# Performance work log

Measured on AMD Instinct MI355X. Metric: run time of the kernel, lower is better.

The kernel has to match this reference:

```python
import jax, jax.numpy as jnp
import numpy as np

N_NODES = 100000
N_EDGES = 6400000
N_IN, E_HID, E_OUT = 768, 512, 256
HID, HEADS, N_CLASSES = 32, 2, 3
NEG_SLOPE = 0.2


def setup_inputs() -> dict:
    key = jax.random.key(0)
    ks = jax.random.split(key, 12)
    def glorot(k, shape):
        fan_in, fan_out = shape[0], shape[-1]
        lim = (6.0 / (fan_in + fan_out)) ** 0.5
        return jax.random.uniform(k, shape, jnp.float32, -lim, lim)
    return {
        "x": jax.random.normal(ks[0], (N_NODES, N_IN), jnp.float32),
        "edge_index": jax.random.randint(ks[1], (2, N_EDGES), 0, N_NODES, jnp.int64),
        "W_e1": glorot(ks[2], (N_IN, E_HID)),
        "b_e1": jnp.zeros((E_HID,), jnp.float32),
        "W_e2": glorot(ks[3], (E_HID, E_OUT)),
        "b_e2": jnp.zeros((E_OUT,), jnp.float32),
        "W_lin": glorot(ks[4], (E_OUT, HID)),
        "b_lin": jnp.zeros((HID,), jnp.float32),
        "W_att": glorot(ks[5], (HID, HEADS * N_CLASSES)),  # GATConv lin (no bias)
        "att_src": glorot(ks[6], (HEADS, N_CLASSES)),
        "att_dst": glorot(ks[7], (HEADS, N_CLASSES)),
        "bias": jnp.zeros((N_CLASSES,), jnp.float32),
    }


def reference(x, edge_index, W_e1, b_e1, W_e2, b_e2, W_lin, b_lin,
              W_att, att_src, att_dst, bias):
    # embedder (Linear-ReLU-Linear) then linear projection to hid
    h = jax.nn.relu(x @ W_e1 + b_e1)
    h = h @ W_e2 + b_e2
    h = h @ W_lin + b_lin                     # [N, hid]
    # GATConv(hid -> n_classes, heads=2, concat=False), add_self_loops=True
    N = h.shape[0]
    hh = (h @ W_att).reshape(N, HEADS, N_CLASSES)      # [N, H, C]
    a_src = jnp.sum(hh * att_src, axis=-1)             # [N, H]
    a_dst = jnp.sum(hh * att_dst, axis=-1)             # [N, H]
    loop = jnp.arange(N, dtype=edge_index.dtype)
    src = jnp.concatenate([edge_index[0], loop])       # [E+N]
    dst = jnp.concatenate([edge_index[1], loop])
    alpha = jax.nn.leaky_relu(a_src[src] + a_dst[dst], NEG_SLOPE)  # [E+N, H]
    # segment softmax over destination node (every segment nonempty via self-loops)
    amax = jax.ops.segment_max(alpha, dst, num_segments=N)
    alpha = jnp.exp(alpha - amax[dst])
    denom = jax.ops.segment_sum(alpha, dst, num_segments=N)
    alpha = alpha / denom[dst]                         # [E+N, H]
    msg = alpha[:, :, None] * hh[src]                  # [E+N, H, C]
    out = jax.ops.segment_sum(msg, dst, num_segments=N)  # [N, H, C]
    return out.mean(axis=1) + bias                     # concat=False -> mean over heads
```

## Files before the change

### kernel.cpp

```cpp
#include <hip/hip_runtime.h>


#define NNODES 100000
#define NEDGES 6400000
#define DIN    768
#define DH1    512
#define DH2    256
#define NEG_SLOPE 0.2f
#define LDSP   40
#define CHUNK  8192
#define NPART  782
#define NBUK   391

typedef __bf16 bf16x8 __attribute__((ext_vector_type(8)));
typedef float  f32x4  __attribute__((ext_vector_type(4)));

__device__ __forceinline__ float bf2f(unsigned short h) {
    return __uint_as_float(((unsigned)h) << 16);
}
__device__ __forceinline__ unsigned short f2bf(float f) {
    unsigned u = __float_as_uint(f);
    unsigned r = u + 0x7FFFu + ((u >> 16) & 1u);
    return (unsigned short)(r >> 16);
}
__device__ __forceinline__ float ldf(const void* p, int i, int isf32) {
    return isf32 ? ((const float*)p)[i] : bf2f(((const unsigned short*)p)[i]);
}
__device__ __forceinline__ uint4 packbf8(const float* p) {
    float4 u = *(const float4*)p;
    float4 v = *(const float4*)(p + 4);
    uint4 r;
    r.x = (unsigned)f2bf(u.x) | ((unsigned)f2bf(u.y) << 16);
    r.y = (unsigned)f2bf(u.z) | ((unsigned)f2bf(u.w) << 16);
    r.z = (unsigned)f2bf(v.x) | ((unsigned)f2bf(v.y) << 16);
    r.w = (unsigned)f2bf(v.z) | ((unsigned)f2bf(v.w) << 16);
    return r;
}

__global__ void detect_dtypes(const unsigned short* x, const unsigned short* we1,
                              const unsigned short* we2, const unsigned short* wlin,
                              const unsigned short* watt, const int* ei, int* flags) {
    __shared__ int cnt;
    int b = blockIdx.x, t = threadIdx.x;
    if (t == 0) cnt = 0;
    __syncthreads();
    if (b < 5) {
        const unsigned short* p = (b == 0) ? x : (b == 1) ? we1 : (b == 2) ? we2
                                  : (b == 3) ? wlin : watt;
        int K = (b == 4) ? 96 : 512;
        int c = 0;
        for (int i = t; i < K; i += 256) {
            int e = (p[2 * i] >> 7) & 0xFF;
            if (e >= 0x66 && e <= 0x8C) c++;
        }
        atomicAdd(&cnt, c);
        __syncthreads();
        if (t == 0) flags[b] = (cnt * 10 < K * 6) ? 1 : 0;
    } else {
        int c = 0;
        for (int i = t; i < 2048; i += 256)
            if (ei[2 * i + 1] != 0) c++;
        atomicAdd(&cnt, c);
        __syncthreads();
        if (t == 0) { flags[5] = (cnt == 0) ? 1 : 0; flags[15] = 0; }
    }
}

__global__ void transpose_conv(const void* in, unsigned short* out, int K, int N,
                               const int* flags, int fidx) {
    int f32 = flags[fidx];
    int idx = blockIdx.x * 256 + threadIdx.x;
    if (idx >= K * N) return;
    int k = idx / N, n = idx - k * N;
    unsigned short v = f32 ? f2bf(((const float*)in)[idx])
                           : ((const unsigned short*)in)[idx];
    out[(size_t)n * K + k] = v;
}

template <bool RELU>
__global__ __launch_bounds__(256)
void gemm_bt(const void* __restrict__ A,
             const unsigned short* __restrict__ Bt,
             const unsigned short* __restrict__ bias,
             unsigned short* __restrict__ C,
             int M, int K, int N, const int* flags, int aidx, int nt_n) {
    __shared__ unsigned short sA[128 * LDSP];
    __shared__ unsigned short sB[128 * LDSP];
    const int af32 = flags[aidx];
    const int tid = threadIdx.x;

    const int nwg = gridDim.x;
    const int bid = blockIdx.x;
    const int xcd = bid & 7, bidx = bid >> 3;
    const int q = nwg >> 3, r = nwg & 7;
    const int logical = (xcd < r ? xcd * (q + 1) : r * (q + 1) + (xcd - r) * q) + bidx;
    const int m0 = (logical / nt_n) * 128;
    const int n0 = (logical % nt_n) * 128;

    const int srow = tid >> 2;
    const int scol = (tid & 3) * 8;
    int ar0 = m0 + srow;      if (ar0 >= M) ar0 = M - 1;
    int ar1 = m0 + 64 + srow; if (ar1 >= M) ar1 = M - 1;
    const unsigned short* Ah = (const unsigned short*)A;
    const float*          Af = (const float*)A;
    const unsigned short* gA0h = Ah + (size_t)ar0 * K + scol;
    const unsigned short* gA1h = Ah + (size_t)ar1 * K + scol;
    const float*          gA0f = Af + (size_t)ar0 * K + scol;
    const float*          gA1f = Af + (size_t)ar1 * K + scol;
    const unsigned short* gB0 = Bt + (size_t)(n0 + srow) * K + scol;
    const unsigned short* gB1 = Bt + (size_t)(n0 + 64 + srow) * K + scol;

    const int wave = tid >> 6, lane = tid & 63;
    const int wr = wave >> 1, wc = wave & 1;
    const int lr = lane & 15;
    const int lk = (lane >> 4) * 8;
    f32x4 acc[4][4] = {};

    for (int k0 = 0; k0 < K; k0 += 32) {
        uint4 a0, a1;
        if (af32) { a0 = packbf8(gA0f + k0); a1 = packbf8(gA1f + k0); }
        else      { a0 = *(const uint4*)(gA0h + k0); a1 = *(const uint4*)(gA1h + k0); }
        uint4 b0 = *(const uint4*)(gB0 + k0);
        uint4 b1 = *(const uint4*)(gB1 + k0);
        __syncthreads();
        *(uint4*)&sA[srow * LDSP + scol]        = a0;
        *(uint4*)&sA[(64 + srow) * LDSP + scol] = a1;
        *(uint4*)&sB[srow * LDSP + scol]        = b0;
        *(uint4*)&sB[(64 + srow) * LDSP + scol] = b1;
        __syncthreads();
        bf16x8 aF[4], bF[4];
#pragma unroll
        for (int i = 0; i < 4; i++) aF[i] = *(const bf16x8*)&sA[(wr * 64 + i * 16 + lr) * LDSP + lk];
#pragma unroll
        for (int j = 0; j < 4; j++) bF[j] = *(const bf16x8*)&sB[(wc * 64 + j * 16 + lr) * LDSP + lk];
#pragma unroll
        for (int i = 0; i < 4; i++)
#pragma unroll
            for (int j = 0; j < 4; j++)
                acc[i][j] = __builtin_amdgcn_mfma_f32_16x16x32_bf16(aF[i], bF[j], acc[i][j], 0, 0, 0);
    }

    float bv[4];
#pragma unroll
    for (int j = 0; j < 4; j++) bv[j] = bf2f(bias[n0 + wc * 64 + j * 16 + lr]);
#pragma unroll
    for (int i = 0; i < 4; i++) {
        int rbase = m0 + wr * 64 + i * 16 + (lane >> 4) * 4;
#pragma unroll
        for (int r = 0; r < 4; r++) {
            int row = rbase + r;
            if (row < M) {
                size_t base = (size_t)row * N + n0 + wc * 64 + lr;
#pragma unroll
                for (int j = 0; j < 4; j++) {
                    float v = acc[i][j][r] + bv[j];
                    if (RELU) v = fmaxf(v, 0.f);
                    C[base + j * 16] = f2bf(v);
                }
            }
        }
    }
}

__global__ __launch_bounds__(256)
void node_att(const unsigned short* __restrict__ h2,
              const void* __restrict__ Wlin,
              const unsigned short* __restrict__ blin,
              const void* __restrict__ Watt,
              const void* __restrict__ attS,
              const void* __restrict__ attD,
              float* __restrict__ hh, float* __restrict__ asrc,
              float* __restrict__ adst, const int* flags) {
    __shared__ float sW[256 * 32];
    __shared__ float sh2[8 * 256];
    __shared__ float sH[8 * 32];
    __shared__ float sHH[8 * 6];
    const int wlf = flags[3], waf = flags[4];
    const int tid = threadIdx.x;
    for (int i = tid; i < 256 * 32; i += 256) sW[i] = ldf(Wlin, i, wlf);
    const int n0 = blockIdx.x * 8;
    {
        int e = tid * 8;
        int r = e >> 8;
        int c = e & 255;
        uint4 v = *(const uint4*)(h2 + (size_t)(n0 + r) * 256 + c);
        float* o = &sh2[r * 256 + c];
        o[0] = __uint_as_float(v.x << 16); o[1] = __uint_as_float(v.x & 0xFFFF0000u);
        o[2] = __uint_as_float(v.y << 16); o[3] = __uint_as_float(v.y & 0xFFFF0000u);
        o[4] = __uint_as_float(v.z << 16); o[5] = __uint_as_float(v.z & 0xFFFF0000u);
        o[6] = __uint_as_float(v.w << 16); o[7] = __uint_as_float(v.w & 0xFFFF0000u);
    }
    __syncthreads();
    const int nl = tid >> 5;
    const int c  = tid & 31;
    float acc = bf2f(blin[c]);
    const float* hrow = &sh2[nl * 256];
#pragma unroll 8
    for (int k = 0; k < 256; k++) acc += hrow[k] * sW[k * 32 + c];
    sH[nl * 32 + c] = acc;
    __syncthreads();
    if (tid < 48) {
        int n = tid / 6, j = tid - (tid / 6) * 6;
        float s = 0.f;
#pragma unroll
        for (int k = 0; k < 32; k++) s += sH[n * 32 + k] * ldf(Watt, k * 6 + j, waf);
        sHH[n * 6 + j] = s;
        hh[(size_t)(n0 + n) * 6 + j] = s;
    }
    __syncthreads();
    if (tid < 16) {
        int n = tid >> 1, hd = tid & 1;
        float s = 0.f, d = 0.f;
#pragma unroll
        for (int cc = 0; cc < 3; cc++) {
            float v = sHH[n * 6 + hd * 3 + cc];
            s += v * ldf(attS, hd * 3 + cc, waf);
            d += v * ldf(attD, hd * 3 + cc, waf);
        }
        asrc[(size_t)(n0 + n) * 2 + hd] = s;
        adst[(size_t)(n0 + n) * 2 + hd] = d;
    }
}


__global__ __launch_bounds__(256)
void part_hist(const int* __restrict__ ei, unsigned* __restrict__ histG,
               const int* __restrict__ flags) {
    __shared__ unsigned h[NBUK];
    int k = blockIdx.x, t = threadIdx.x;
    for (int i = t; i < NBUK; i += 256) h[i] = 0;
    __syncthreads();
    int e0 = k * CHUNK;
    int e1 = e0 + CHUNK; if (e1 > NEDGES) e1 = NEDGES;
    int i64 = flags[5];
    for (int e = e0 + t; e < e1; e += 256) {
        int d = i64 ? (int)((const long long*)ei)[NEDGES + e] : ei[NEDGES + e];
        atomicAdd(&h[d >> 8], 1u);
    }
    __syncthreads();
    for (int i = t; i < NBUK; i += 256) histG[(size_t)i * NPART + k] = h[i];
}

__global__ __launch_bounds__(256)
void part_scan(const unsigned* __restrict__ histG, unsigned* __restrict__ start,
               unsigned* __restrict__ btot) {
    int b = blockIdx.x, t = threadIdx.x;
    const unsigned* col = histG + (size_t)b * NPART;
    unsigned* out = start + (size_t)b * NPART;
    unsigned v[4]; unsigned sum = 0;
#pragma unroll
    for (int i = 0; i < 4; i++) {
        int k = t * 4 + i;
        unsigned x = (k < NPART) ? col[k] : 0;
        v[i] = x; sum += x;
    }
    __shared__ unsigned s[256];
    s[t] = sum; __syncthreads();
    for (int off = 1; off < 256; off <<= 1) {
        unsigned x = (t >= off) ? s[t - off] : 0;
        __syncthreads();
        s[t] += x;
        __syncthreads();
    }
    unsigned ex = s[t] - sum;
    unsigned run = ex;
#pragma unroll
    for (int i = 0; i < 4; i++) {
        int k = t * 4 + i;
        if (k < NPART) out[k] = run;
        run += v[i];
    }
    if (t == 255) btot[b] = s[255];
}

__global__ void bucket_base(const unsigned* __restrict__ btot, unsigned* __restrict__ bbase) {
    __shared__ unsigned s[512];
    int t = threadIdx.x;
    unsigned v = (t < NBUK) ? btot[t] : 0;
    s[t] = v;
    __syncthreads();
    for (int off = 1; off < 512; off <<= 1) {
        unsigned x = (t >= off) ? s[t - off] : 0;
        __syncthreads();
        s[t] += x;
        __syncthreads();
    }
    if (t < NBUK) bbase[t] = s[t] - v;
    if (t == NBUK - 1) bbase[NBUK] = s[t];
}

__global__ __launch_bounds__(256)
void part_scatter(const int* __restrict__ ei, const unsigned* __restrict__ start,
                  const unsigned* __restrict__ bbase, uint2* __restrict__ pairs,
                  const int* __restrict__ flags) {
    __shared__ unsigned cur[NBUK];
    int k = blockIdx.x, t = threadIdx.x;
    for (int i = t; i < NBUK; i += 256)
        cur[i] = bbase[i] + start[(size_t)i * NPART + k];
    __syncthreads();
    int e0 = k * CHUNK;
    int e1 = e0 + CHUNK; if (e1 > NEDGES) e1 = NEDGES;
    int i64 = flags[5];
    for (int e = e0 + t; e < e1; e += 256) {
        int s, d;
        if (i64) {
            const long long* E = (const long long*)ei;
            s = (int)E[e];
            d = (int)E[NEDGES + e];
        } else {
            s = ei[e];
            d = ei[NEDGES + e];
        }
        unsigned pos = atomicAdd(&cur[d >> 8], 1u);
        pairs[pos] = make_uint2((unsigned)s, (unsigned)d);
    }
}

__global__ __launch_bounds__(256)
void bucket_csr(const uint2* __restrict__ pairs, const unsigned* __restrict__ bbase,
                int* __restrict__ count, int* __restrict__ offs,
                int* __restrict__ sorted) {
    int b = blockIdx.x, t = threadIdx.x;
    unsigned e0 = bbase[b], e1 = bbase[b + 1];
    int d0n = b << 8;
    int nd = NNODES - d0n; if (nd > 256) nd = 256;
    __shared__ unsigned cnt[256], s[256], cur[256];
    cnt[t] = 0;
    __syncthreads();
    for (unsigned e = e0 + t; e < e1; e += 256)
        atomicAdd(&cnt[pairs[e].y & 255], 1u);
    __syncthreads();
    unsigned myc = cnt[t];
    s[t] = myc; __syncthreads();
    for (int off = 1; off < 256; off <<= 1) {
        unsigned x = (t >= off) ? s[t - off] : 0;
        __syncthreads();
        s[t] += x;
        __syncthreads();
    }
    unsigned ex = s[t] - myc;
    if (t < nd) {
        count[d0n + t] = (int)myc;
        offs[d0n + t]  = (int)(e0 + ex);
    }
    cur[t] = e0 + ex;
    __syncthreads();
    for (unsigned e = e0 + t; e < e1; e += 256) {
        uint2 p = pairs[e];
        unsigned pos = atomicAdd(&cur[p.y & 255], 1u);
        sorted[pos] = (int)p.x;
    }
}

__global__ __launch_bounds__(256)
void gather_finalize(const int* __restrict__ sorted, const int* __restrict__ offs,
                     const int* __restrict__ count,
                     const float* __restrict__ asrc, const float* __restrict__ adst,
                     const float* __restrict__ hh,
                     const unsigned short* __restrict__ bias,
                     void* __restrict__ out, const int* __restrict__ flags) {
    int w = blockIdx.x * 4 + (threadIdx.x >> 6);
    if (w >= NNODES) return;
    int lane = threadIdx.x & 63;
    int base = offs[w];
    int cnt  = count[w];
    float2 ad = *(const float2*)(adst + 2 * (size_t)w);

    float d0 = 0.f, d1 = 0.f;
    float n0 = 0.f, n1 = 0.f, n2 = 0.f, n3 = 0.f, n4 = 0.f, n5 = 0.f;
    for (int k = lane; k < cnt; k += 64) {
        int s = sorted[base + k];
        float2 as = *(const float2*)(asrc + 2 * (size_t)s);
        float a0 = as.x + ad.x; a0 = a0 > 0.f ? a0 : NEG_SLOPE * a0;
        float a1 = as.y + ad.y; a1 = a1 > 0.f ? a1 : NEG_SLOPE * a1;
        float p0 = __expf(fminf(a0, 60.f));
        float p1 = __expf(fminf(a1, 60.f));
        const float* hs = hh + 6 * (size_t)s;
        d0 += p0; d1 += p1;
        n0 += p0 * hs[0]; n1 += p0 * hs[1]; n2 += p0 * hs[2];
        n3 += p1 * hs[3]; n4 += p1 * hs[4]; n5 += p1 * hs[5];
    }
#pragma unroll
    for (int m = 32; m > 0; m >>= 1) {
        d0 += __shfl_xor(d0, m, 64); d1 += __shfl_xor(d1, m, 64);
        n0 += __shfl_xor(n0, m, 64); n1 += __shfl_xor(n1, m, 64);
        n2 += __shfl_xor(n2, m, 64); n3 += __shfl_xor(n3, m, 64);
        n4 += __shfl_xor(n4, m, 64); n5 += __shfl_xor(n5, m, 64);
    }
    if (lane == 0) {
        float2 as = *(const float2*)(asrc + 2 * (size_t)w);
        float a0 = as.x + ad.x; a0 = a0 > 0.f ? a0 : NEG_SLOPE * a0;
        float a1 = as.y + ad.y; a1 = a1 > 0.f ? a1 : NEG_SLOPE * a1;
        float p0 = __expf(fminf(a0, 60.f));
        float p1 = __expf(fminf(a1, 60.f));
        const float* hw = hh + 6 * (size_t)w;
        d0 += p0; d1 += p1;
        n0 += p0 * hw[0]; n1 += p0 * hw[1]; n2 += p0 * hw[2];
        n3 += p1 * hw[3]; n4 += p1 * hw[4]; n5 += p1 * hw[5];

        float o0 = 0.5f * (n0 / d0 + n3 / d1) + bf2f(bias[0]);
        float o1 = 0.5f * (n1 / d0 + n4 / d1) + bf2f(bias[1]);
        float o2 = 0.5f * (n2 / d0 + n5 / d1) + bf2f(bias[2]);
        if (flags[0]) {
            float* o = (float*)out;
            o[3 * (size_t)w + 0] = o0; o[3 * (size_t)w + 1] = o1; o[3 * (size_t)w + 2] = o2;
        } else {
            unsigned short* o = (unsigned short*)out;
            o[3 * (size_t)w + 0] = f2bf(o0); o[3 * (size_t)w + 1] = f2bf(o1); o[3 * (size_t)w + 2] = f2bf(o2);
        }
    }
}

extern "C" void kernel_launch(void* const* d_in, const int* in_sizes, int n_in,
                              void* d_out, int out_size, void* d_ws, size_t ws_size,
                              hipStream_t stream) {
    const unsigned short* x    = (const unsigned short*)d_in[0];
    const int*            ei   = (const int*)d_in[1];
    const unsigned short* We1  = (const unsigned short*)d_in[2];
    const unsigned short* be1  = (const unsigned short*)d_in[3];
    const unsigned short* We2  = (const unsigned short*)d_in[4];
    const unsigned short* be2  = (const unsigned short*)d_in[5];
    const unsigned short* Wlin = (const unsigned short*)d_in[6];
    const unsigned short* blin = (const unsigned short*)d_in[7];
    const unsigned short* Watt = (const unsigned short*)d_in[8];
    const unsigned short* attS = (const unsigned short*)d_in[9];
    const unsigned short* attD = (const unsigned short*)d_in[10];
    const unsigned short* bias = (const unsigned short*)d_in[11];

    char* ws = (char*)d_ws;
    unsigned short* W1t   = (unsigned short*)(ws + 0);
    unsigned short* W2t   = (unsigned short*)(ws + 786432);
    unsigned short* h2    = (unsigned short*)(ws + 1048576);
    float*    hh    = (float*)(ws + 52248576);
    float*    asrc  = (float*)(ws + 54648576);
    float*    adst  = (float*)(ws + 55448576);
    int*      count = (int*)(ws + 56248576);
    int*      offs  = (int*)(ws + 56648576);
    unsigned* btot  = (unsigned*)(ws + 57048576);
    unsigned* bbase = (unsigned*)(ws + 57052672);
    int*      flags = (int*)(ws + 59448576);
    unsigned short* h1 = (unsigned short*)(ws + 59448640);
    uint2*    pairs  = (uint2*)(ws + 59448640);
    int*      sorted = (int*)(ws + 110648640);
    unsigned* histG  = (unsigned*)(ws + 136248640);
    unsigned* start  = (unsigned*)(ws + 137471744);
    (void)ws_size; (void)in_sizes; (void)n_in; (void)out_size;

    detect_dtypes<<<6, 256, 0, stream>>>(x, We1, We2, Wlin, Watt, ei, flags);

    transpose_conv<<<(DIN * DH1 + 255) / 256, 256, 0, stream>>>(We1, W1t, DIN, DH1, flags, 1);
    transpose_conv<<<(DH1 * DH2 + 255) / 256, 256, 0, stream>>>(We2, W2t, DH1, DH2, flags, 2);

    dim3 blk(256);
    int nwg1 = ((NNODES + 127) / 128) * (DH1 / 128);
    gemm_bt<true><<<nwg1, blk, 0, stream>>>(x, W1t, be1, h1, NNODES, DIN, DH1,
                                            flags, 0, DH1 / 128);
    int nwg2 = ((NNODES + 127) / 128) * (DH2 / 128);
    gemm_bt<false><<<nwg2, blk, 0, stream>>>(h1, W2t, be2, h2, NNODES, DH1, DH2,
                                             flags, 15, DH2 / 128);

    node_att<<<NNODES / 8, 256, 0, stream>>>(h2, Wlin, blin, Watt, attS, attD,
                                             hh, asrc, adst, flags);

    part_hist<<<NPART, 256, 0, stream>>>(ei, histG, flags);
    part_scan<<<NBUK, 256, 0, stream>>>(histG, start, btot);
    bucket_base<<<1, 512, 0, stream>>>(btot, bbase);
    part_scatter<<<NPART, 256, 0, stream>>>(ei, start, bbase, pairs, flags);
    bucket_csr<<<NBUK, 256, 0, stream>>>(pairs, bbase, count, offs, sorted);
    gather_finalize<<<(NNODES + 3) / 4, 256, 0, stream>>>(sorted, offs, count,
                                                          asrc, adst, hh, bias,
                                                          d_out, flags);
}
```

Baseline: 1.061 ms.

## Replace CSR sort with bucket LDS-atomic accumulation and use direct-to-LDS GEMM loads

The per-destination CSR build (bucket_csr) and the gather kernel are replaced by bucket_acc. It accumulates softmax numerators and denominators in shared-memory atomics per 256-node bucket, splits each bucket across 8 sub-blocks, and merges the partial sums in combine_out. Edge pairs are packed into one 32-bit word (src<<8 | local dst), and the per-node source data is packed into an 8-float record so a gather needs two float4 loads. The bf16 GEMM path now uses global_load_lds to copy tiles straight into a k-major LDS layout. In exchange it adds LDS atomic contention and a partial buffer of 8×N×8 floats that must be written and reduced.

```diff
diff --git a/kernel.cpp b/kernel.cpp
--- a/kernel.cpp
+++ b/kernel.cpp
@@ -7,10 +7,10 @@
 #define DH1    512
 #define DH2    256
 #define NEG_SLOPE 0.2f
-#define LDSP   40
 #define CHUNK  8192
 #define NPART  782
 #define NBUK   391
+#define SSUB   8
 
 typedef __bf16 bf16x8 __attribute__((ext_vector_type(8)));
 typedef float  f32x4  __attribute__((ext_vector_type(4)));
@@ -35,6 +35,11 @@
     r.z = (unsigned)f2bf(v.x) | ((unsigned)f2bf(v.y) << 16);
     r.w = (unsigned)f2bf(v.z) | ((unsigned)f2bf(v.w) << 16);
     return r;
+}
+__device__ __forceinline__ void gload16(const unsigned short* g, unsigned short* l) {
+    __builtin_amdgcn_global_load_lds(
+        (const __attribute__((address_space(1))) unsigned int*)g,
+        (__attribute__((address_space(3))) unsigned int*)l, 16, 0, 0);
 }
 
 __global__ void detect_dtypes(const unsigned short* x, const unsigned short* we1,
@@ -84,8 +89,8 @@
              const unsigned short* __restrict__ bias,
              unsigned short* __restrict__ C,
              int M, int K, int N, const int* flags, int aidx, int nt_n) {
-    __shared__ unsigned short sA[128 * LDSP];
-    __shared__ unsigned short sB[128 * LDSP];
+    __shared__ unsigned short sA[4096];
+    __shared__ unsigned short sB[4096];
     const int af32 = flags[aidx];
     const int tid = threadIdx.x;
 
@@ -97,42 +102,53 @@
     const int m0 = (logical / nt_n) * 128;
     const int n0 = (logical % nt_n) * 128;
 
+    const int wave = tid >> 6, lane = tid & 63;
+
     const int srow = tid >> 2;
-    const int scol = (tid & 3) * 8;
+    const int c4   = tid & 3;
     int ar0 = m0 + srow;      if (ar0 >= M) ar0 = M - 1;
     int ar1 = m0 + 64 + srow; if (ar1 >= M) ar1 = M - 1;
-    const unsigned short* Ah = (const unsigned short*)A;
-    const float*          Af = (const float*)A;
-    const unsigned short* gA0h = Ah + (size_t)ar0 * K + scol;
-    const unsigned short* gA1h = Ah + (size_t)ar1 * K + scol;
-    const float*          gA0f = Af + (size_t)ar0 * K + scol;
-    const float*          gA1f = Af + (size_t)ar1 * K + scol;
-    const unsigned short* gB0 = Bt + (size_t)(n0 + srow) * K + scol;
-    const unsigned short* gB1 = Bt + (size_t)(n0 + 64 + srow) * K + scol;
-
-    const int wave = tid >> 6, lane = tid & 63;
+    const float* gA0f = (const float*)A + (size_t)ar0 * K + c4 * 8;
+    const float* gA1f = (const float*)A + (size_t)ar1 * K + c4 * 8;
+    unsigned short* swA0 = &sA[(c4 * 128 + srow) * 8];
+    unsigned short* swA1 = &sA[(c4 * 128 + 64 + srow) * 8];
+
+    const int grow = ((wave & 1) << 6) + lane;
+    int arow = m0 + grow; if (arow >= M) arow = M - 1;
+    const unsigned short* gAl1 = (const unsigned short*)A + (size_t)arow * K + (wave >> 1) * 8;
+    const unsigned short* gAl2 = gAl1 + 16;
+    const unsigned short* gBl1 = Bt + (size_t)(n0 + grow) * K + (wave >> 1) * 8;
+    const unsigned short* gBl2 = gBl1 + 16;
+    unsigned short* ldsA1 = &sA[wave * 512];
+    unsigned short* ldsA2 = &sA[2048 + wave * 512];
+    unsigned short* ldsB1 = &sB[wave * 512];
+    unsigned short* ldsB2 = &sB[2048 + wave * 512];
+
     const int wr = wave >> 1, wc = wave & 1;
     const int lr = lane & 15;
-    const int lk = (lane >> 4) * 8;
+    const int aBase = ((lane >> 4) * 128 + wr * 64 + lr) * 8;
+    const int bBase = ((lane >> 4) * 128 + wc * 64 + lr) * 8;
     f32x4 acc[4][4] = {};
 
     for (int k0 = 0; k0 < K; k0 += 32) {
         uint4 a0, a1;
         if (af32) { a0 = packbf8(gA0f + k0); a1 = packbf8(gA1f + k0); }
-        else      { a0 = *(const uint4*)(gA0h + k0); a1 = *(const uint4*)(gA1h + k0); }
-        uint4 b0 = *(const uint4*)(gB0 + k0);
-        uint4 b1 = *(const uint4*)(gB1 + k0);
-        __syncthreads();
-        *(uint4*)&sA[srow * LDSP + scol]        = a0;
-        *(uint4*)&sA[(64 + srow) * LDSP + scol] = a1;
-        *(uint4*)&sB[srow * LDSP + scol]        = b0;
-        *(uint4*)&sB[(64 + srow) * LDSP + scol] = b1;
+        __syncthreads();
+        if (af32) {
+            *(uint4*)swA0 = a0;
+            *(uint4*)swA1 = a1;
+        } else {
+            gload16(gAl1 + k0, ldsA1);
+            gload16(gAl2 + k0, ldsA2);
+        }
+        gload16(gBl1 + k0, ldsB1);
+        gload16(gBl2 + k0, ldsB2);
         __syncthreads();
         bf16x8 aF[4], bF[4];
 #pragma unroll
-        for (int i = 0; i < 4; i++) aF[i] = *(const bf16x8*)&sA[(wr * 64 + i * 16 + lr) * LDSP + lk];
-#pragma unroll
-        for (int j = 0; j < 4; j++) bF[j] = *(const bf16x8*)&sB[(wc * 64 + j * 16 + lr) * LDSP + lk];
+        for (int i = 0; i < 4; i++) aF[i] = *(const bf16x8*)&sA[aBase + i * 128];
+#pragma unroll
+        for (int j = 0; j < 4; j++) bF[j] = *(const bf16x8*)&sB[bBase + j * 128];
 #pragma unroll
         for (int i = 0; i < 4; i++)
 #pragma unroll
@@ -147,13 +163,13 @@
     for (int i = 0; i < 4; i++) {
         int rbase = m0 + wr * 64 + i * 16 + (lane >> 4) * 4;
 #pragma unroll
-        for (int r = 0; r < 4; r++) {
-            int row = rbase + r;
+        for (int r2 = 0; r2 < 4; r2++) {
+            int row = rbase + r2;
             if (row < M) {
                 size_t base = (size_t)row * N + n0 + wc * 64 + lr;
 #pragma unroll
                 for (int j = 0; j < 4; j++) {
-                    float v = acc[i][j][r] + bv[j];
+                    float v = acc[i][j][r2] + bv[j];
                     if (RELU) v = fmaxf(v, 0.f);
                     C[base + j * 16] = f2bf(v);
                 }
@@ -169,8 +185,8 @@
               const void* __restrict__ Watt,
               const void* __restrict__ attS,
               const void* __restrict__ attD,
-              float* __restrict__ hh, float* __restrict__ asrc,
-              float* __restrict__ adst, const int* flags) {
+              float* __restrict__ spack, float* __restrict__ adst,
+              const int* flags) {
     __shared__ float sW[256 * 32];
     __shared__ float sh2[8 * 256];
     __shared__ float sH[8 * 32];
@@ -205,7 +221,6 @@
 #pragma unroll
         for (int k = 0; k < 32; k++) s += sH[n * 32 + k] * ldf(Watt, k * 6 + j, waf);
         sHH[n * 6 + j] = s;
-        hh[(size_t)(n0 + n) * 6 + j] = s;
     }
     __syncthreads();
     if (tid < 16) {
@@ -217,8 +232,12 @@
             s += v * ldf(attS, hd * 3 + cc, waf);
             d += v * ldf(attD, hd * 3 + cc, waf);
         }
-        asrc[(size_t)(n0 + n) * 2 + hd] = s;
         adst[(size_t)(n0 + n) * 2 + hd] = d;
+        spack[(size_t)(n0 + n) * 8 + hd] = s;
+    }
+    if (tid < 48) {
+        int n = tid / 6, j = tid - (tid / 6) * 6;
+        spack[(size_t)(n0 + n) * 8 + 2 + j] = sHH[n * 6 + j];
     }
 }
 
@@ -291,7 +310,7 @@
 
 __global__ __launch_bounds__(256)
 void part_scatter(const int* __restrict__ ei, const unsigned* __restrict__ start,
-                  const unsigned* __restrict__ bbase, uint2* __restrict__ pairs,
+                  const unsigned* __restrict__ bbase, unsigned* __restrict__ pairs,
                   const int* __restrict__ flags) {
     __shared__ unsigned cur[NBUK];
     int k = blockIdx.x, t = threadIdx.x;
@@ -312,102 +331,81 @@
             d = ei[NEDGES + e];
         }
         unsigned pos = atomicAdd(&cur[d >> 8], 1u);
-        pairs[pos] = make_uint2((unsigned)s, (unsigned)d);
-    }
-}
-
-__global__ __launch_bounds__(256)
-void bucket_csr(const uint2* __restrict__ pairs, const unsigned* __restrict__ bbase,
-                int* __restrict__ count, int* __restrict__ offs,
-                int* __restrict__ sorted) {
-    int b = blockIdx.x, t = threadIdx.x;
-    unsigned e0 = bbase[b], e1 = bbase[b + 1];
+        pairs[pos] = ((unsigned)s << 8) | (unsigned)(d & 255);
+    }
+}
+
+__global__ __launch_bounds__(256)
+void bucket_acc(const unsigned* __restrict__ pairs, const unsigned* __restrict__ bbase,
+                const float* __restrict__ spack, const float* __restrict__ adst,
+                float* __restrict__ partial) {
+    __shared__ float acc[256 * 8];
+    __shared__ float sad[512];
+    int b = blockIdx.x, s = blockIdx.y, t = threadIdx.x;
     int d0n = b << 8;
     int nd = NNODES - d0n; if (nd > 256) nd = 256;
-    __shared__ unsigned cnt[256], s[256], cur[256];
-    cnt[t] = 0;
-    __syncthreads();
-    for (unsigned e = e0 + t; e < e1; e += 256)
-        atomicAdd(&cnt[pairs[e].y & 255], 1u);
-    __syncthreads();
-    unsigned myc = cnt[t];
-    s[t] = myc; __syncthreads();
-    for (int off = 1; off < 256; off <<= 1) {
-        unsigned x = (t >= off) ? s[t - off] : 0;
-        __syncthreads();
-        s[t] += x;
-        __syncthreads();
-    }
-    unsigned ex = s[t] - myc;
-    if (t < nd) {
-        count[d0n + t] = (int)myc;
-        offs[d0n + t]  = (int)(e0 + ex);
-    }
-    cur[t] = e0 + ex;
-    __syncthreads();
-    for (unsigned e = e0 + t; e < e1; e += 256) {
-        uint2 p = pairs[e];
-        unsigned pos = atomicAdd(&cur[p.y & 255], 1u);
-        sorted[pos] = (int)p.x;
-    }
-}
-
-__global__ __launch_bounds__(256)
-void gather_finalize(const int* __restrict__ sorted, const int* __restrict__ offs,
-                     const int* __restrict__ count,
-                     const float* __restrict__ asrc, const float* __restrict__ adst,
-                     const float* __restrict__ hh,
-                     const unsigned short* __restrict__ bias,
-                     void* __restrict__ out, const int* __restrict__ flags) {
-    int w = blockIdx.x * 4 + (threadIdx.x >> 6);
-    if (w >= NNODES) return;
-    int lane = threadIdx.x & 63;
-    int base = offs[w];
-    int cnt  = count[w];
-    float2 ad = *(const float2*)(adst + 2 * (size_t)w);
-
-    float d0 = 0.f, d1 = 0.f;
-    float n0 = 0.f, n1 = 0.f, n2 = 0.f, n3 = 0.f, n4 = 0.f, n5 = 0.f;
-    for (int k = lane; k < cnt; k += 64) {
-        int s = sorted[base + k];
-        float2 as = *(const float2*)(asrc + 2 * (size_t)s);
-        float a0 = as.x + ad.x; a0 = a0 > 0.f ? a0 : NEG_SLOPE * a0;
-        float a1 = as.y + ad.y; a1 = a1 > 0.f ? a1 : NEG_SLOPE * a1;
+    for (int i = t; i < 2048; i += 256) acc[i] = 0.f;
+    for (int i = t; i < 2 * nd; i += 256) sad[i] = adst[(size_t)d0n * 2 + i];
+    unsigned e0 = bbase[b], e1 = bbase[b + 1];
+    unsigned per = (e1 - e0 + SSUB - 1) / SSUB;
+    unsigned s0 = e0 + s * per;
+    unsigned s1 = s0 + per; if (s1 > e1) s1 = e1;
+    __syncthreads();
+    for (unsigned e = s0 + t; e < s1; e += 256) {
+        unsigned p = pairs[e];
+        unsigned src = p >> 8, dl = p & 255u;
+        float4 q0 = *(const float4*)(spack + 8 * (size_t)src);
+        float4 q1 = *(const float4*)(spack + 8 * (size_t)src + 4);
+        float a0 = q0.x + sad[2 * dl];     a0 = a0 > 0.f ? a0 : NEG_SLOPE * a0;
+        float a1 = q0.y + sad[2 * dl + 1]; a1 = a1 > 0.f ? a1 : NEG_SLOPE * a1;
         float p0 = __expf(fminf(a0, 60.f));
         float p1 = __expf(fminf(a1, 60.f));
-        const float* hs = hh + 6 * (size_t)s;
-        d0 += p0; d1 += p1;
-        n0 += p0 * hs[0]; n1 += p0 * hs[1]; n2 += p0 * hs[2];
-        n3 += p1 * hs[3]; n4 += p1 * hs[4]; n5 += p1 * hs[5];
-    }
-#pragma unroll
-    for (int m = 32; m > 0; m >>= 1) {
-        d0 += __shfl_xor(d0, m, 64); d1 += __shfl_xor(d1, m, 64);
-        n0 += __shfl_xor(n0, m, 64); n1 += __shfl_xor(n1, m, 64);
-        n2 += __shfl_xor(n2, m, 64); n3 += __shfl_xor(n3, m, 64);
-        n4 += __shfl_xor(n4, m, 64); n5 += __shfl_xor(n5, m, 64);
-    }
-    if (lane == 0) {
-        float2 as = *(const float2*)(asrc + 2 * (size_t)w);
-        float a0 = as.x + ad.x; a0 = a0 > 0.f ? a0 : NEG_SLOPE * a0;
-        float a1 = as.y + ad.y; a1 = a1 > 0.f ? a1 : NEG_SLOPE * a1;
-        float p0 = __expf(fminf(a0, 60.f));
-        float p1 = __expf(fminf(a1, 60.f));
-        const float* hw = hh + 6 * (size_t)w;
-        d0 += p0; d1 += p1;
-        n0 += p0 * hw[0]; n1 += p0 * hw[1]; n2 += p0 * hw[2];
-        n3 += p1 * hw[3]; n4 += p1 * hw[4]; n5 += p1 * hw[5];
-
-        float o0 = 0.5f * (n0 / d0 + n3 / d1) + bf2f(bias[0]);
-        float o1 = 0.5f * (n1 / d0 + n4 / d1) + bf2f(bias[1]);
-        float o2 = 0.5f * (n2 / d0 + n5 / d1) + bf2f(bias[2]);
-        if (flags[0]) {
-            float* o = (float*)out;
-            o[3 * (size_t)w + 0] = o0; o[3 * (size_t)w + 1] = o1; o[3 * (size_t)w + 2] = o2;
-        } else {
-            unsigned short* o = (unsigned short*)out;
-            o[3 * (size_t)w + 0] = f2bf(o0); o[3 * (size_t)w + 1] = f2bf(o1); o[3 * (size_t)w + 2] = f2bf(o2);
-        }
+        float* a = &acc[dl * 8];
+        atomicAdd(&a[0], p0);
+        atomicAdd(&a[1], p1);
+        atomicAdd(&a[2], p0 * q0.z);
+        atomicAdd(&a[3], p0 * q0.w);
+        atomicAdd(&a[4], p0 * q1.x);
+        atomicAdd(&a[5], p1 * q1.y);
+        atomicAdd(&a[6], p1 * q1.z);
+        atomicAdd(&a[7], p1 * q1.w);
+    }
+    __syncthreads();
+    float* dst = partial + ((size_t)s * NNODES + d0n) * 8;
+    for (int i = t; i < nd * 8; i += 256) dst[i] = acc[i];
+}
+
+__global__ void combine_out(const float* __restrict__ partial, const float* __restrict__ spack,
+                            const float* __restrict__ adst,
+                            const unsigned short* __restrict__ bias,
+                            void* __restrict__ out, const int* __restrict__ flags) {
+    int n = blockIdx.x * 256 + threadIdx.x;
+    if (n >= NNODES) return;
+    float v[8] = {0.f, 0.f, 0.f, 0.f, 0.f, 0.f, 0.f, 0.f};
+    for (int s = 0; s < SSUB; s++) {
+        const float* p = partial + ((size_t)s * NNODES + n) * 8;
+#pragma unroll
+        for (int j = 0; j < 8; j++) v[j] += p[j];
+    }
+    float4 q0 = *(const float4*)(spack + 8 * (size_t)n);
+    float4 q1 = *(const float4*)(spack + 8 * (size_t)n + 4);
+    float2 ad = *(const float2*)(adst + 2 * (size_t)n);
+    float a0 = q0.x + ad.x; a0 = a0 > 0.f ? a0 : NEG_SLOPE * a0;
+    float a1 = q0.y + ad.y; a1 = a1 > 0.f ? a1 : NEG_SLOPE * a1;
+    float p0 = __expf(fminf(a0, 60.f));
+    float p1 = __expf(fminf(a1, 60.f));
+    v[0] += p0; v[1] += p1;
+    v[2] += p0 * q0.z; v[3] += p0 * q0.w; v[4] += p0 * q1.x;
+    v[5] += p1 * q1.y; v[6] += p1 * q1.z; v[7] += p1 * q1.w;
+    float o0 = 0.5f * (v[2] / v[0] + v[5] / v[1]) + bf2f(bias[0]);
+    float o1 = 0.5f * (v[3] / v[0] + v[6] / v[1]) + bf2f(bias[1]);
+    float o2 = 0.5f * (v[4] / v[0] + v[7] / v[1]) + bf2f(bias[2]);
+    if (flags[0]) {
+        float* o = (float*)out;
+        o[3 * (size_t)n + 0] = o0; o[3 * (size_t)n + 1] = o1; o[3 * (size_t)n + 2] = o2;
+    } else {
+        unsigned short* o = (unsigned short*)out;
+        o[3 * (size_t)n + 0] = f2bf(o0); o[3 * (size_t)n + 1] = f2bf(o1); o[3 * (size_t)n + 2] = f2bf(o2);
     }
 }
 
@@ -431,19 +429,16 @@
     unsigned short* W1t   = (unsigned short*)(ws + 0);
     unsigned short* W2t   = (unsigned short*)(ws + 786432);
     unsigned short* h2    = (unsigned short*)(ws + 1048576);
-    float*    hh    = (float*)(ws + 52248576);
-    float*    asrc  = (float*)(ws + 54648576);
+    float*    spack = (float*)(ws + 52248576);
     float*    adst  = (float*)(ws + 55448576);
-    int*      count = (int*)(ws + 56248576);
-    int*      offs  = (int*)(ws + 56648576);
     unsigned* btot  = (unsigned*)(ws + 57048576);
     unsigned* bbase = (unsigned*)(ws + 57052672);
     int*      flags = (int*)(ws + 59448576);
     unsigned short* h1 = (unsigned short*)(ws + 59448640);
-    uint2*    pairs  = (uint2*)(ws + 59448640);
-    int*      sorted = (int*)(ws + 110648640);
-    unsigned* histG  = (unsigned*)(ws + 136248640);
-    unsigned* start  = (unsigned*)(ws + 137471744);
+    unsigned* pairs   = (unsigned*)(ws + 59448640);
+    float*    partial = (float*)(ws + 85048640);
+    unsigned* histG   = (unsigned*)(ws + 136248640);
+    unsigned* start   = (unsigned*)(ws + 137471744);
     (void)ws_size; (void)in_sizes; (void)n_in; (void)out_size;
 
     detect_dtypes<<<6, 256, 0, stream>>>(x, We1, We2, Wlin, Watt, ei, flags);
@@ -460,14 +455,13 @@
                                              flags, 15, DH2 / 128);
 
     node_att<<<NNODES / 8, 256, 0, stream>>>(h2, Wlin, blin, Watt, attS, attD,
-                                             hh, asrc, adst, flags);
+                                             spack, adst, flags);
 
     part_hist<<<NPART, 256, 0, stream>>>(ei, histG, flags);
     part_scan<<<NBUK, 256, 0, stream>>>(histG, start, btot);
     bucket_base<<<1, 512, 0, stream>>>(btot, bbase);
     part_scatter<<<NPART, 256, 0, stream>>>(ei, start, bbase, pairs, flags);
-    bucket_csr<<<NBUK, 256, 0, stream>>>(pairs, bbase, count, offs, sorted);
-    gather_finalize<<<(NNODES + 3) / 4, 256, 0, stream>>>(sorted, offs, count,
-                                                          asrc, adst, hh, bias,
-                                                          d_out, flags);
-}
+    bucket_acc<<<dim3(NBUK, SSUB), 256, 0, stream>>>(pairs, bbase, spack, adst, partial);
+    combine_out<<<(NNODES + 255) / 256, 256, 0, stream>>>(partial, spack, adst,
+                                                          bias, d_out, flags);
+}
```

Result: slower. 1.240 ms (+16.8%).
